# Optimization experiments

Measured on AMD Instinct MI355X. Metric: run time of the kernel, lower is better.

Reference implementation:

```python
import jax, jax.numpy as jnp
import numpy as np

B = 8          # number of subgraphs (seq_start_end rows)
N = 2048       # nodes per subgraph (equal-size segments)
D = 64         # h_dim
H = 4          # gat_heads
ALPHA = 0.2    # leaky relu slope


def setup_inputs() -> dict:
    key = jax.random.key(0)
    k1, k2, k3, k4, k5 = jax.random.split(key, 5)
    h_states = jax.random.normal(k1, (B * N, D), dtype=jnp.float32)
    # xavier-ish scales
    W_heads = jax.random.normal(k2, (H, D, D), dtype=jnp.float32) * (1.414 * np.sqrt(2.0 / (D + D)))
    a_heads = jax.random.normal(k3, (H, 2 * D), dtype=jnp.float32) * (1.414 * np.sqrt(2.0 / (2 * D + 1)))
    W_out = jax.random.normal(k4, (H * D, D), dtype=jnp.float32) * (1.414 * np.sqrt(2.0 / (H * D + D)))
    a_out = jax.random.normal(k5, (2 * D,), dtype=jnp.float32) * (1.414 * np.sqrt(2.0 / (2 * D + 1)))
    starts = jnp.arange(B, dtype=jnp.int32) * N
    seq_start_end = jnp.stack([starts, starts + N], axis=1)  # (B, 2)
    return {"h_states": h_states, "W_heads": W_heads, "a_heads": a_heads,
            "W_out": W_out, "a_out": a_out, "seq_start_end": seq_start_end}


def _gat_layer(x, W, a):
    """Dense GAT layer. Equivalent to the torch.cat O(N^2*2d) construction,
    rewritten as separate a1/a2 projections + broadcast add. Eval mode (no dropout)."""
    h = x @ W                      # (N, dout)
    d = W.shape[1]
    s1 = h @ a[:d]                 # (N,)  score contribution of source node i
    s2 = h @ a[d:]                 # (N,)  score contribution of target node j
    e = jax.nn.leaky_relu(s1[:, None] + s2[None, :], ALPHA)  # (N, N)
    attn = jax.nn.softmax(e, axis=1)
    return attn @ h                # (N, dout)


def reference(h_states, W_heads, a_heads, W_out, a_out, seq_start_end):
    # seq_start_end encodes B equal contiguous segments of length N -> reshape
    x = h_states.reshape(B, N, D)

    def per_graph(xg):  # xg: (N, D)
        # multi-head attention layers, concat=True -> elu on each head output
        hp = jax.vmap(lambda W, a: jax.nn.elu(_gat_layer(xg, W, a)))(W_heads, a_heads)  # (H, N, D)
        xc = jnp.transpose(hp, (1, 0, 2)).reshape(N, H * D)
        # output attention layer, concat=False (no elu inside), then elu + log_softmax outside
        out = jax.nn.elu(_gat_layer(xc, W_out, a_out))   # (N, D)
        return jax.nn.log_softmax(out, axis=1)

    return jax.vmap(per_graph)(x).reshape(B * N, D)
```

## Files before the change

### kernel.cpp

```cpp
#include <hip/hip_runtime.h>
#include <math.h>

#define NTOT 16384
#define NSEG 2048
#define TROW 65
#define TSTRIDE 133120ull
#define CSTRIDE 8385ull

#define OFF_HH   0ull
#define OFF_XC   4194304ull
#define OFF_S1H  8388608ull
#define OFF_S2H  8454144ull
#define OFF_S1O  8519680ull
#define OFF_S2O  8536064ull
#define OFF_SVAL 8552448ull
#define OFF_WN   8617984ull
#define OFF_SIDX 8683520ull
#define OFF_CA   8749056ull
#define OFF_CS   9017376ull
#define OFF_A    9285696ull
#define OFF_S    13545536ull

__device__ inline unsigned long long pack_key(float v, int idx) {
    unsigned u = __float_as_uint(v);
    u = (u & 0x80000000u) ? ~u : (u | 0x80000000u);
    return ((unsigned long long)u << 32) | (unsigned)idx;
}
__device__ inline float unpack_key(unsigned long long k) {
    unsigned u = (unsigned)(k >> 32);
    u = (u & 0x80000000u) ? (u ^ 0x80000000u) : ~u;
    return __uint_as_float(u);
}
__device__ inline unsigned long long shfl_xor_u64(unsigned long long x, int mask) {
    unsigned lo = (unsigned)x, hi = (unsigned)(x >> 32);
    lo = (unsigned)__shfl_xor((int)lo, mask, 64);
    hi = (unsigned)__shfl_xor((int)hi, mask, 64);
    return ((unsigned long long)hi << 32) | lo;
}

__global__ __launch_bounds__(256) void gemm1_k(const float* __restrict__ X,
                                               const float* __restrict__ Wh,
                                               const float* __restrict__ aH,
                                               float* __restrict__ hh,
                                               float* __restrict__ s1h,
                                               float* __restrict__ s2h) {
    __shared__ float As[64][68];
    __shared__ float Bs[64][68];
    const int tid = threadIdx.x;
    const int bm = blockIdx.x, h = blockIdx.y;
    const int c0 = tid & 63, r0 = tid >> 6;
#pragma unroll
    for (int r = 0; r < 16; ++r) {
        int row = r0 + r * 4;
        As[c0][row] = X[(size_t)(bm * 64 + row) * 64 + c0];
        Bs[row][c0] = Wh[h * 4096 + row * 64 + c0];
    }
    __syncthreads();
    const int tx = tid & 15, ty = tid >> 4;
    const int m0 = ty * 4, n0 = tx * 4;
    float acc[4][4] = {};
#pragma unroll
    for (int kk = 0; kk < 64; ++kk) {
        float4 a = *(const float4*)&As[kk][m0];
        float4 b = *(const float4*)&Bs[kk][n0];
        acc[0][0] += a.x * b.x; acc[0][1] += a.x * b.y; acc[0][2] += a.x * b.z; acc[0][3] += a.x * b.w;
        acc[1][0] += a.y * b.x; acc[1][1] += a.y * b.y; acc[1][2] += a.y * b.z; acc[1][3] += a.y * b.w;
        acc[2][0] += a.z * b.x; acc[2][1] += a.z * b.y; acc[2][2] += a.z * b.z; acc[2][3] += a.z * b.w;
        acc[3][0] += a.w * b.x; acc[3][1] += a.w * b.y; acc[3][2] += a.w * b.z; acc[3][3] += a.w * b.w;
    }
#pragma unroll
    for (int i = 0; i < 4; ++i) {
        float4 v = make_float4(acc[i][0], acc[i][1], acc[i][2], acc[i][3]);
        *(float4*)&hh[(size_t)(bm * 64 + m0 + i) * 256 + h * 64 + n0] = v;
    }
#pragma unroll
    for (int i = 0; i < 4; ++i) {
        float p1 = 0.f, p2 = 0.f;
#pragma unroll
        for (int jj = 0; jj < 4; ++jj) {
            p1 += acc[i][jj] * aH[h * 128 + n0 + jj];
            p2 += acc[i][jj] * aH[h * 128 + 64 + n0 + jj];
        }
#pragma unroll
        for (int off = 8; off; off >>= 1) {
            p1 += __shfl_xor(p1, off, 16);
            p2 += __shfl_xor(p2, off, 16);
        }
        if (tx == 0) {
            s1h[h * NTOT + bm * 64 + m0 + i] = p1;
            s2h[h * NTOT + bm * 64 + m0 + i] = p2;
        }
    }
}

__global__ __launch_bounds__(256) void gemm2_k(const float* __restrict__ XC,
                                               const float* __restrict__ Wo,
                                               const float* __restrict__ aO,
                                               float* __restrict__ hc,
                                               float* __restrict__ s1o,
                                               float* __restrict__ s2o) {
    __shared__ float As[64][34];
    __shared__ float Bs[64][68];
    const int tid = threadIdx.x;
    const int bm = blockIdx.x;
    const int c0 = tid & 63, r0 = tid >> 6;
    const int tx = tid & 15, ty = tid >> 4;
    const int m0 = ty * 2, n0 = tx * 4;
    float acc[2][4] = {};
    for (int kt = 0; kt < 4; ++kt) {
#pragma unroll
        for (int r = 0; r < 8; ++r) {
            int row = r0 + r * 4;
            As[c0][row] = XC[(size_t)(bm * 32 + row) * 256 + kt * 64 + c0];
        }
#pragma unroll
        for (int r = 0; r < 16; ++r) {
            int row = r0 + r * 4;
            Bs[row][c0] = Wo[(kt * 64 + row) * 64 + c0];
        }
        __syncthreads();
#pragma unroll
        for (int kk = 0; kk < 64; ++kk) {
            float2 a = *(const float2*)&As[kk][m0];
            float4 b = *(const float4*)&Bs[kk][n0];
            acc[0][0] += a.x * b.x; acc[0][1] += a.x * b.y; acc[0][2] += a.x * b.z; acc[0][3] += a.x * b.w;
            acc[1][0] += a.y * b.x; acc[1][1] += a.y * b.y; acc[1][2] += a.y * b.z; acc[1][3] += a.y * b.w;
        }
        __syncthreads();
    }
#pragma unroll
    for (int i = 0; i < 2; ++i) {
        float4 v = make_float4(acc[i][0], acc[i][1], acc[i][2], acc[i][3]);
        *(float4*)&hc[(size_t)(bm * 32 + m0 + i) * 64 + n0] = v;
    }
#pragma unroll
    for (int i = 0; i < 2; ++i) {
        float p1 = 0.f, p2 = 0.f;
#pragma unroll
        for (int jj = 0; jj < 4; ++jj) {
            p1 += acc[i][jj] * aO[n0 + jj];
            p2 += acc[i][jj] * aO[64 + n0 + jj];
        }
#pragma unroll
        for (int off = 8; off; off >>= 1) {
            p1 += __shfl_xor(p1, off, 16);
            p2 += __shfl_xor(p2, off, 16);
        }
        if (tx == 0) {
            s1o[bm * 32 + m0 + i] = p1;
            s2o[bm * 32 + m0 + i] = p2;
        }
    }
}

__global__ __launch_bounds__(1024) void sort_k(const float* __restrict__ s2_all,
                                               int heads,
                                               float* __restrict__ g_sval,
                                               int* __restrict__ g_sidx,
                                               float* __restrict__ g_wN) {
    __shared__ unsigned long long sA[2][1024];
    __shared__ unsigned long long sB[2][1024];
    __shared__ float sM2;
    const int tid = threadIdx.x, t = blockIdx.x;
    const int g = t / heads, h = t % heads;
    const float* s2p = s2_all + (size_t)h * NTOT + (size_t)g * NSEG;

    unsigned long long a0 = pack_key(s2p[tid], tid);
    unsigned long long a1 = pack_key(s2p[tid + 1024], tid + 1024);
    int p = 0;
    for (int k = 2; k <= 2048; k <<= 1) {
        const bool up0 = (tid & k) == 0;
        const bool up1 = (((tid + 1024) & k) == 0);
        for (int j = k >> 1; j > 0; j >>= 1) {
            if (j >= 1024) {
                unsigned long long lo = a0 < a1 ? a0 : a1;
                unsigned long long hi = a0 < a1 ? a1 : a0;
                a0 = up0 ? lo : hi;
                a1 = up0 ? hi : lo;
            } else if (j >= 64) {
                sA[p][tid] = a0; sB[p][tid] = a1;
                __syncthreads();
                unsigned long long q0 = sA[p][tid ^ j], q1 = sB[p][tid ^ j];
                bool lower = (tid & j) == 0;
                a0 = ((a0 < q0) == (lower == up0)) ? a0 : q0;
                a1 = ((a1 < q1) == (lower == up1)) ? a1 : q1;
                p ^= 1;
            } else {
                unsigned long long q0 = shfl_xor_u64(a0, j);
                unsigned long long q1 = shfl_xor_u64(a1, j);
                bool lower = (tid & j) == 0;
                a0 = ((a0 < q0) == (lower == up0)) ? a0 : q0;
                a1 = ((a1 < q1) == (lower == up1)) ? a1 : q1;
            }
        }
    }
    float v0 = unpack_key(a0), v1 = unpack_key(a1);
    if (tid == 1023) sM2 = v1;
    __syncthreads();
    const float M2 = sM2;
    int i0 = (int)(unsigned)(a0 & 0xffffffffu);
    int i1 = (int)(unsigned)(a1 & 0xffffffffu);
    float w0 = __expf(0.2f * (v0 - M2));
    float w1 = __expf(0.2f * (v1 - M2));
    size_t o = (size_t)t * NSEG;
    g_sval[o + tid] = v0; g_sval[o + tid + 1024] = v1;
    g_sidx[o + tid] = i0; g_sidx[o + tid + 1024] = i1;
    g_wN[o + tid] = w0;   g_wN[o + tid + 1024] = w1;
}

__global__ __launch_bounds__(256) void tabw_k(const float* __restrict__ V,
                                              int heads, int vstride,
                                              const int* __restrict__ g_sidx,
                                              const float* __restrict__ g_wN,
                                              float* __restrict__ g_A, float* __restrict__ g_S,
                                              float* __restrict__ g_TA, float* __restrict__ g_TS) {
    const int t = blockIdx.y, g = t / heads, h = t % heads;
    const int wv = threadIdx.x >> 6, lane = threadIdx.x & 63;
    const int c = blockIdx.x * 4 + wv;
    const int base = c * 16;
    const float* Vp = V + (size_t)g * NSEG * vstride + h * 64;
    const int* sidx = g_sidx + (size_t)t * NSEG + base;
    const float* wnp = g_wN + (size_t)t * NSEG + base;
    float wn[16], vv[16];
#pragma unroll
    for (int j = 0; j < 16; ++j) wn[j] = wnp[j];
#pragma unroll
    for (int j = 0; j < 16; ++j) vv[j] = Vp[(size_t)sidx[j] * vstride + lane];
    float* A = g_A + (size_t)t * TSTRIDE;
    float* S = g_S + (size_t)t * TSTRIDE;
    float accA = 0.f, scaA = 0.f;
#pragma unroll
    for (int j = 0; j < 16; ++j) {
        size_t pos = base + j;
        A[pos * TROW + lane] = accA;
        if (lane == 0) A[pos * TROW + 64] = scaA;
        accA += wn[j] * vv[j]; scaA += wn[j];
    }
    g_TA[((size_t)t * 128 + c) * TROW + lane] = accA;
    if (lane == 0) g_TA[((size_t)t * 128 + c) * TROW + 64] = scaA;
    float accS = 0.f, scaS = 0.f;
#pragma unroll
    for (int j = 15; j >= 0; --j) {
        float w = wn[j], w2 = w * w, wp = w2 * w2 * w;
        accS += wp * vv[j]; scaS += wp;
        size_t pos = base + j;
        S[pos * TROW + lane] = accS;
        if (lane == 0) S[pos * TROW + 64] = scaS;
    }
    g_TS[((size_t)t * 128 + c) * TROW + lane] = accS;
    if (lane == 0) g_TS[((size_t)t * 128 + c) * TROW + 64] = scaS;
}

__global__ __launch_bounds__(256) void scan_k(const float* __restrict__ g_TA,
                                              const float* __restrict__ g_TS,
                                              float* __restrict__ g_CA,
                                              float* __restrict__ g_CS) {
    const int t = blockIdx.x, tid = threadIdx.x;
    if (tid < 65) {
        const float* TA = g_TA + (size_t)t * 128 * TROW + tid;
        float* CA = g_CA + (size_t)t * CSTRIDE + tid;
        float run = 0.f;
#pragma unroll 4
        for (int c = 0; c < 128; ++c) { CA[c * TROW] = run; run += TA[c * TROW]; }
        CA[128 * TROW] = run;
    } else if (tid >= 128 && tid < 193) {
        const int d = tid - 128;
        const float* TS = g_TS + (size_t)t * 128 * TROW + d;
        float* CS = g_CS + (size_t)t * CSTRIDE + d;
        float run = 0.f;
#pragma unroll 4
        for (int c = 127; c >= 0; --c) { CS[c * TROW] = run; run += TS[c * TROW]; }
    }
}

template <int MODE>
__global__ __launch_bounds__(256) void query_k(const float* __restrict__ s1_all,
                                               float* __restrict__ out,
                                               int heads, int ostride,
                                               const float* __restrict__ g_sval,
                                               const float* __restrict__ g_A,
                                               const float* __restrict__ g_S,
                                               const float* __restrict__ g_CA,
                                               const float* __restrict__ g_CS) {
    __shared__ float sval[NSEG];
    const int tid = threadIdx.x;
    const int t = blockIdx.y, g = t / heads, h = t % heads;
    const float4* sv4 = (const float4*)(g_sval + (size_t)t * NSEG);
    for (int i = tid; i < NSEG / 4; i += 256) ((float4*)sval)[i] = sv4[i];
    __syncthreads();
    const float M2 = sval[NSEG - 1];
    const int lane = tid & 63, wv = tid >> 6;
    const int q0 = blockIdx.x * 64 + wv * 16;
    const float* s1p = s1_all + (size_t)h * NTOT + (size_t)g * NSEG;
    float* outp = out + (size_t)g * NSEG * ostride + h * 64;
    const float* A = g_A + (size_t)t * TSTRIDE;
    const float* S = g_S + (size_t)t * TSTRIDE;
    const float* CA = g_CA + (size_t)t * CSTRIDE;
    const float* CS = g_CS + (size_t)t * CSTRIDE;
    int myq = q0 + (lane & 15);
    float s1v = s1p[myq];
    float th = -s1v;
    int lo = 0, hi = NSEG;
    while (lo < hi) { int mid = (lo + hi) >> 1; if (sval[mid] <= th) lo = mid + 1; else hi = mid; }
#pragma unroll 4
    for (int j = 0; j < 16; ++j) {
        int k = __shfl(lo, j, 64);
        float s1q = __shfl(s1v, j, 64);
        float accA, scaA, accS, scaS;
        if (k < NSEG) {
            const int c = k >> 4;
            const float* rowA = A + (size_t)k * TROW;
            const float* rowS = S + (size_t)k * TROW;
            const float* rowCA = CA + (size_t)c * TROW;
            const float* rowCS = CS + (size_t)c * TROW;
            accA = rowA[lane] + rowCA[lane]; scaA = rowA[64] + rowCA[64];
            accS = rowS[lane] + rowCS[lane]; scaS = rowS[64] + rowCS[64];
        } else {
            accA = CA[128 * TROW + lane]; scaA = CA[128 * TROW + 64];
            accS = 0.f; scaS = 0.f;
        }
        float cc = __expf(-0.8f * fmaxf(s1q + M2, 0.f));
        float o = (accS + cc * accA) / (scaS + cc * scaA);
        o = o > 0.f ? o : expm1f(o);
        int q = q0 + j;
        if (MODE == 0) {
            outp[(size_t)q * ostride + lane] = o;
        } else {
            float m = o;
#pragma unroll
            for (int off = 32; off; off >>= 1) m = fmaxf(m, __shfl_xor(m, off, 64));
            float e = __expf(o - m);
#pragma unroll
            for (int off = 32; off; off >>= 1) e += __shfl_xor(e, off, 64);
            outp[(size_t)q * ostride + lane] = o - m - __logf(e);
        }
    }
}

extern "C" void kernel_launch(void* const* d_in, const int* in_sizes, int n_in,
                              void* d_out, int out_size, void* d_ws, size_t ws_size,
                              hipStream_t stream) {
    const float* h_states = (const float*)d_in[0];
    const float* W_heads = (const float*)d_in[1];
    const float* a_heads = (const float*)d_in[2];
    const float* W_out = (const float*)d_in[3];
    const float* a_out = (const float*)d_in[4];
    float* w = (float*)d_ws;
    float* hh = w + OFF_HH;
    float* xc = w + OFF_XC;
    float* hc = w + OFF_HH;
    float* s1h = w + OFF_S1H;
    float* s2h = w + OFF_S2H;
    float* s1o = w + OFF_S1O;
    float* s2o = w + OFF_S2O;
    float* g_sval = w + OFF_SVAL;
    float* g_wN = w + OFF_WN;
    int* g_sidx = (int*)(w + OFF_SIDX);
    float* g_TA = w + OFF_XC;
    float* g_TS = w + OFF_XC + 266240;
    float* g_CA = w + OFF_CA;
    float* g_CS = w + OFF_CS;
    float* g_A = w + OFF_A;
    float* g_S = w + OFF_S;
    float* outp = (float*)d_out;

    gemm1_k<<<dim3(256, 4), 256, 0, stream>>>(h_states, W_heads, a_heads, hh, s1h, s2h);
    sort_k<<<32, 1024, 0, stream>>>(s2h, 4, g_sval, g_sidx, g_wN);
    tabw_k<<<dim3(32, 32), 256, 0, stream>>>(hh, 4, 256, g_sidx, g_wN, g_A, g_S, g_TA, g_TS);
    scan_k<<<32, 256, 0, stream>>>(g_TA, g_TS, g_CA, g_CS);
    query_k<0><<<dim3(32, 32), 256, 0, stream>>>(s1h, xc, 4, 256, g_sval, g_A, g_S, g_CA, g_CS);
    gemm2_k<<<512, 256, 0, stream>>>(xc, W_out, a_out, hc, s1o, s2o);
    sort_k<<<8, 1024, 0, stream>>>(s2o, 1, g_sval, g_sidx, g_wN);
    tabw_k<<<dim3(32, 8), 256, 0, stream>>>(hc, 1, 64, g_sidx, g_wN, g_A, g_S, g_TA, g_TS);
    scan_k<<<8, 256, 0, stream>>>(g_TA, g_TS, g_CA, g_CS);
    query_k<1><<<dim3(32, 8), 256, 0, stream>>>(s1o, outp, 1, 64, g_sval, g_A, g_S, g_CA, g_CS);
}
```

Before: 202.0 us.

## Interleave prefix/suffix tables, split scalar sums, remap blocks per XCD

The A and S prefix tables, previously two arrays with 65-float rows, now share one 128-float-aligned row per position. The scalar weight sums move to separate arrays, so vector loads are aligned and one row serves both directions. gemm1 now writes per-head hidden states contiguously by (head, graph), giving tabw_k dense 64-wide rows to gather. tabw_k and query_k map block IDs so that all blocks of one task land on the same XCD, for L2 locality. The risk is that the index arithmetic must match the gemm2 output layout and the workspace offsets must not overlap.

```diff
diff --git a/kernel.cpp b/kernel.cpp
--- a/kernel.cpp
+++ b/kernel.cpp
@@ -3,9 +3,6 @@
 
 #define NTOT 16384
 #define NSEG 2048
-#define TROW 65
-#define TSTRIDE 133120ull
-#define CSTRIDE 8385ull
 
 #define OFF_HH   0ull
 #define OFF_XC   4194304ull
@@ -16,10 +13,12 @@
 #define OFF_SVAL 8552448ull
 #define OFF_WN   8617984ull
 #define OFF_SIDX 8683520ull
-#define OFF_CA   8749056ull
-#define OFF_CS   9017376ull
-#define OFF_A    9285696ull
-#define OFF_S    13545536ull
+#define OFF_VAS  8749056ull
+#define OFF_CSA  9277440ull
+#define OFF_CSS  9281568ull
+#define OFF_SCA  9285696ull
+#define OFF_SCS  9351232ull
+#define OFF_AS   9416768ull
 
 __device__ inline unsigned long long pack_key(float v, int idx) {
     unsigned u = __float_as_uint(v);
@@ -68,10 +67,12 @@
         acc[2][0] += a.z * b.x; acc[2][1] += a.z * b.y; acc[2][2] += a.z * b.z; acc[2][3] += a.z * b.w;
         acc[3][0] += a.w * b.x; acc[3][1] += a.w * b.y; acc[3][2] += a.w * b.z; acc[3][3] += a.w * b.w;
     }
+    const int g = bm >> 5;
+    const int nb = (bm * 64) & 2047;
 #pragma unroll
     for (int i = 0; i < 4; ++i) {
         float4 v = make_float4(acc[i][0], acc[i][1], acc[i][2], acc[i][3]);
-        *(float4*)&hh[(size_t)(bm * 64 + m0 + i) * 256 + h * 64 + n0] = v;
+        *(float4*)&hh[(((size_t)h * 8 + g) * NSEG + nb + m0 + i) * 64 + n0] = v;
     }
 #pragma unroll
     for (int i = 0; i < 4; ++i) {
@@ -209,94 +210,112 @@
 }
 
 __global__ __launch_bounds__(256) void tabw_k(const float* __restrict__ V,
-                                              int heads, int vstride,
+                                              int heads, int ntask,
                                               const int* __restrict__ g_sidx,
                                               const float* __restrict__ g_wN,
-                                              float* __restrict__ g_A, float* __restrict__ g_S,
-                                              float* __restrict__ g_TA, float* __restrict__ g_TS) {
-    const int t = blockIdx.y, g = t / heads, h = t % heads;
+                                              float* __restrict__ AS,
+                                              float* __restrict__ SCA, float* __restrict__ SCS,
+                                              float* __restrict__ TAS,
+                                              float* __restrict__ TSA, float* __restrict__ TSS) {
+    const int L = blockIdx.x + (int)(gridDim.x * blockIdx.y);
+    const int xcd = L & 7, slot = L >> 3;
+    const int tpx = ntask >> 3;
+    const int t = xcd * tpx + (slot >> 5);
+    const int u = slot & 31;
     const int wv = threadIdx.x >> 6, lane = threadIdx.x & 63;
-    const int c = blockIdx.x * 4 + wv;
-    const int base = c * 16;
-    const float* Vp = V + (size_t)g * NSEG * vstride + h * 64;
+    const int c = u * 4 + wv, base = c * 16;
+    const int g = t / heads, h = t % heads;
+    const int seg = h * (ntask / heads) + g;
+    const float* Vp = V + (size_t)seg * NSEG * 64;
     const int* sidx = g_sidx + (size_t)t * NSEG + base;
     const float* wnp = g_wN + (size_t)t * NSEG + base;
     float wn[16], vv[16];
 #pragma unroll
     for (int j = 0; j < 16; ++j) wn[j] = wnp[j];
 #pragma unroll
-    for (int j = 0; j < 16; ++j) vv[j] = Vp[(size_t)sidx[j] * vstride + lane];
-    float* A = g_A + (size_t)t * TSTRIDE;
-    float* S = g_S + (size_t)t * TSTRIDE;
+    for (int j = 0; j < 16; ++j) vv[j] = Vp[(size_t)sidx[j] * 64 + lane];
+    float* ASp = AS + (size_t)t * NSEG * 128;
     float accA = 0.f, scaA = 0.f;
 #pragma unroll
     for (int j = 0; j < 16; ++j) {
         size_t pos = base + j;
-        A[pos * TROW + lane] = accA;
-        if (lane == 0) A[pos * TROW + 64] = scaA;
+        ASp[pos * 128 + lane] = accA;
+        if (lane == 0) SCA[(size_t)t * NSEG + pos] = scaA;
         accA += wn[j] * vv[j]; scaA += wn[j];
     }
-    g_TA[((size_t)t * 128 + c) * TROW + lane] = accA;
-    if (lane == 0) g_TA[((size_t)t * 128 + c) * TROW + 64] = scaA;
+    TAS[((size_t)t * 128 + c) * 128 + lane] = accA;
+    if (lane == 0) TSA[t * 128 + c] = scaA;
     float accS = 0.f, scaS = 0.f;
 #pragma unroll
     for (int j = 15; j >= 0; --j) {
         float w = wn[j], w2 = w * w, wp = w2 * w2 * w;
         accS += wp * vv[j]; scaS += wp;
         size_t pos = base + j;
-        S[pos * TROW + lane] = accS;
-        if (lane == 0) S[pos * TROW + 64] = scaS;
-    }
-    g_TS[((size_t)t * 128 + c) * TROW + lane] = accS;
-    if (lane == 0) g_TS[((size_t)t * 128 + c) * TROW + 64] = scaS;
-}
-
-__global__ __launch_bounds__(256) void scan_k(const float* __restrict__ g_TA,
-                                              const float* __restrict__ g_TS,
-                                              float* __restrict__ g_CA,
-                                              float* __restrict__ g_CS) {
+        ASp[pos * 128 + 64 + lane] = accS;
+        if (lane == 0) SCS[(size_t)t * NSEG + pos] = scaS;
+    }
+    TAS[((size_t)t * 128 + c) * 128 + 64 + lane] = accS;
+    if (lane == 0) TSS[t * 128 + c] = scaS;
+}
+
+__global__ __launch_bounds__(256) void scan_k(const float* __restrict__ TAS,
+                                              const float* __restrict__ TSA,
+                                              const float* __restrict__ TSS,
+                                              float* __restrict__ VAS,
+                                              float* __restrict__ CSA, float* __restrict__ CSS) {
     const int t = blockIdx.x, tid = threadIdx.x;
-    if (tid < 65) {
-        const float* TA = g_TA + (size_t)t * 128 * TROW + tid;
-        float* CA = g_CA + (size_t)t * CSTRIDE + tid;
+    const float* T = TAS + (size_t)t * 128 * 128;
+    float* Vo = VAS + (size_t)t * 129 * 128;
+    if (tid < 64) {
         float run = 0.f;
 #pragma unroll 4
-        for (int c = 0; c < 128; ++c) { CA[c * TROW] = run; run += TA[c * TROW]; }
-        CA[128 * TROW] = run;
-    } else if (tid >= 128 && tid < 193) {
-        const int d = tid - 128;
-        const float* TS = g_TS + (size_t)t * 128 * TROW + d;
-        float* CS = g_CS + (size_t)t * CSTRIDE + d;
+        for (int c = 0; c < 128; ++c) { Vo[c * 128 + tid] = run; run += T[c * 128 + tid]; }
+        Vo[128 * 128 + tid] = run;
+    } else if (tid < 128) {
         float run = 0.f;
 #pragma unroll 4
-        for (int c = 127; c >= 0; --c) { CS[c * TROW] = run; run += TS[c * TROW]; }
+        for (int c = 127; c >= 0; --c) { Vo[c * 128 + tid] = run; run += T[c * 128 + tid]; }
+    } else if (tid == 128) {
+        float run = 0.f;
+        for (int c = 0; c < 128; ++c) { CSA[t * 129 + c] = run; run += TSA[t * 128 + c]; }
+        CSA[t * 129 + 128] = run;
+    } else if (tid == 129) {
+        float run = 0.f;
+        for (int c = 127; c >= 0; --c) { CSS[t * 129 + c] = run; run += TSS[t * 128 + c]; }
     }
 }
 
 template <int MODE>
 __global__ __launch_bounds__(256) void query_k(const float* __restrict__ s1_all,
                                                float* __restrict__ out,
-                                               int heads, int ostride,
+                                               int heads, int ntask, int ostride,
                                                const float* __restrict__ g_sval,
-                                               const float* __restrict__ g_A,
-                                               const float* __restrict__ g_S,
-                                               const float* __restrict__ g_CA,
-                                               const float* __restrict__ g_CS) {
+                                               const float* __restrict__ AS,
+                                               const float* __restrict__ SCA, const float* __restrict__ SCS,
+                                               const float* __restrict__ VAS,
+                                               const float* __restrict__ CSA, const float* __restrict__ CSS) {
     __shared__ float sval[NSEG];
     const int tid = threadIdx.x;
-    const int t = blockIdx.y, g = t / heads, h = t % heads;
+    const int L = blockIdx.x + (int)(gridDim.x * blockIdx.y);
+    const int xcd = L & 7, slot = L >> 3;
+    const int tpx = ntask >> 3;
+    const int t = xcd * tpx + (slot >> 5);
+    const int u = slot & 31;
+    const int g = t / heads, h = t % heads;
     const float4* sv4 = (const float4*)(g_sval + (size_t)t * NSEG);
     for (int i = tid; i < NSEG / 4; i += 256) ((float4*)sval)[i] = sv4[i];
     __syncthreads();
     const float M2 = sval[NSEG - 1];
     const int lane = tid & 63, wv = tid >> 6;
-    const int q0 = blockIdx.x * 64 + wv * 16;
+    const int q0 = u * 64 + wv * 16;
     const float* s1p = s1_all + (size_t)h * NTOT + (size_t)g * NSEG;
     float* outp = out + (size_t)g * NSEG * ostride + h * 64;
-    const float* A = g_A + (size_t)t * TSTRIDE;
-    const float* S = g_S + (size_t)t * TSTRIDE;
-    const float* CA = g_CA + (size_t)t * CSTRIDE;
-    const float* CS = g_CS + (size_t)t * CSTRIDE;
+    const float* ASp = AS + (size_t)t * NSEG * 128;
+    const float* VASp = VAS + (size_t)t * 129 * 128;
+    const float* scA = SCA + (size_t)t * NSEG;
+    const float* scS = SCS + (size_t)t * NSEG;
+    const float* csA = CSA + (size_t)t * 129;
+    const float* csS = CSS + (size_t)t * 129;
     int myq = q0 + (lane & 15);
     float s1v = s1p[myq];
     float th = -s1v;
@@ -309,14 +328,14 @@
         float accA, scaA, accS, scaS;
         if (k < NSEG) {
             const int c = k >> 4;
-            const float* rowA = A + (size_t)k * TROW;
-            const float* rowS = S + (size_t)k * TROW;
-            const float* rowCA = CA + (size_t)c * TROW;
-            const float* rowCS = CS + (size_t)c * TROW;
-            accA = rowA[lane] + rowCA[lane]; scaA = rowA[64] + rowCA[64];
-            accS = rowS[lane] + rowCS[lane]; scaS = rowS[64] + rowCS[64];
+            const float* rowP = ASp + (size_t)k * 128;
+            const float* rowC = VASp + (size_t)c * 128;
+            accA = rowP[lane] + rowC[lane];
+            accS = rowP[64 + lane] + rowC[64 + lane];
+            scaA = scA[k] + csA[c];
+            scaS = scS[k] + csS[c];
         } else {
-            accA = CA[128 * TROW + lane]; scaA = CA[128 * TROW + 64];
+            accA = VASp[128 * 128 + lane]; scaA = csA[128];
             accS = 0.f; scaS = 0.f;
         }
         float cc = __expf(-0.8f * fmaxf(s1q + M2, 0.f));
@@ -356,22 +375,25 @@
     float* g_sval = w + OFF_SVAL;
     float* g_wN = w + OFF_WN;
     int* g_sidx = (int*)(w + OFF_SIDX);
-    float* g_TA = w + OFF_XC;
-    float* g_TS = w + OFF_XC + 266240;
-    float* g_CA = w + OFF_CA;
-    float* g_CS = w + OFF_CS;
-    float* g_A = w + OFF_A;
-    float* g_S = w + OFF_S;
+    float* TAS = w + OFF_XC;
+    float* TSA = w + OFF_XC + 524288;
+    float* TSS = w + OFF_XC + 528384;
+    float* VAS = w + OFF_VAS;
+    float* CSA = w + OFF_CSA;
+    float* CSS = w + OFF_CSS;
+    float* SCA = w + OFF_SCA;
+    float* SCS = w + OFF_SCS;
+    float* AS = w + OFF_AS;
     float* outp = (float*)d_out;
 
     gemm1_k<<<dim3(256, 4), 256, 0, stream>>>(h_states, W_heads, a_heads, hh, s1h, s2h);
     sort_k<<<32, 1024, 0, stream>>>(s2h, 4, g_sval, g_sidx, g_wN);
-    tabw_k<<<dim3(32, 32), 256, 0, stream>>>(hh, 4, 256, g_sidx, g_wN, g_A, g_S, g_TA, g_TS);
-    scan_k<<<32, 256, 0, stream>>>(g_TA, g_TS, g_CA, g_CS);
-    query_k<0><<<dim3(32, 32), 256, 0, stream>>>(s1h, xc, 4, 256, g_sval, g_A, g_S, g_CA, g_CS);
+    tabw_k<<<dim3(32, 32), 256, 0, stream>>>(hh, 4, 32, g_sidx, g_wN, AS, SCA, SCS, TAS, TSA, TSS);
+    scan_k<<<32, 256, 0, stream>>>(TAS, TSA, TSS, VAS, CSA, CSS);
+    query_k<0><<<dim3(32, 32), 256, 0, stream>>>(s1h, xc, 4, 32, 256, g_sval, AS, SCA, SCS, VAS, CSA, CSS);
     gemm2_k<<<512, 256, 0, stream>>>(xc, W_out, a_out, hc, s1o, s2o);
     sort_k<<<8, 1024, 0, stream>>>(s2o, 1, g_sval, g_sidx, g_wN);
-    tabw_k<<<dim3(32, 8), 256, 0, stream>>>(hc, 1, 64, g_sidx, g_wN, g_A, g_S, g_TA, g_TS);
-    scan_k<<<8, 256, 0, stream>>>(g_TA, g_TS, g_CA, g_CS);
-    query_k<1><<<dim3(32, 8), 256, 0, stream>>>(s1o, outp, 1, 64, g_sval, g_A, g_S, g_CA, g_CS);
-}
+    tabw_k<<<dim3(32, 8), 256, 0, stream>>>(hc, 1, 8, g_sidx, g_wN, AS, SCA, SCS, TAS, TSA, TSS);
+    scan_k<<<8, 256, 0, stream>>>(TAS, TSA, TSS, VAS, CSA, CSS);
+    query_k<1><<<dim3(32, 8), 256, 0, stream>>>(s1o, outp, 1, 8, 64, g_sval, AS, SCA, SCS, VAS, CSA, CSS);
+}
```

Measured after the change: 199.4 us. No clear change (-1.3%).
